# Performance work log

Measured on AMD Instinct MI355X. Metric: run time of the kernel, lower is better.

The kernel has to match this reference:

```python
import jax, jax.numpy as jnp
from jax import lax
import numpy as np

B, T, H, V, C = 64, 64, 1024, 32000, 10
Z, CD = 32, 8  # latent dim, cond embedding dim


def lstm_scan(x_tbh, h0, c0, Wih, Whh, bih, bhh):
    """PyTorch-convention LSTM over time. x_tbh: [T,B,H]; returns hs [T,B,H]."""
    def step(carry, x):
        h, c = carry
        gates = x @ Wih.T + bih + h @ Whh.T + bhh  # [B,4H]
        i, f, g, o = jnp.split(gates, 4, axis=-1)
        c = jax.nn.sigmoid(f) * c + jax.nn.sigmoid(i) * jnp.tanh(g)
        h = jax.nn.sigmoid(o) * jnp.tanh(c)
        return (h, c), h
    _, hs = lax.scan(step, (h0, c0), x_tbh)
    return hs


def setup_inputs() -> dict:
    key = jax.random.key(0)
    ks = jax.random.split(key, 24)
    s = 0.02
    d = {
        'input_word': jax.random.randint(ks[0], (B, T), 0, V),
        'cond': jax.random.randint(ks[1], (B,), 0, C),
        'emb_N': jax.random.normal(ks[2], (V, H), jnp.float32) * s,
        'Wih_N': jax.random.normal(ks[3], (4 * H, H), jnp.float32) * s,
        'Whh_N': jax.random.normal(ks[4], (4 * H, H), jnp.float32) * s,
        'bih_N': jnp.zeros((4 * H,), jnp.float32),
        'bhh_N': jnp.zeros((4 * H,), jnp.float32),
        'emb_D': jax.random.normal(ks[5], (V, H), jnp.float32) * s,
        'Wih_D': jax.random.normal(ks[6], (4 * H, H), jnp.float32) * s,
        'Whh_D': jax.random.normal(ks[7], (4 * H, H), jnp.float32) * s,
        'bih_D': jnp.zeros((4 * H,), jnp.float32),
        'bhh_D': jnp.zeros((4 * H,), jnp.float32),
        'emb_cond': jax.random.normal(ks[8], (C, CD), jnp.float32) * s,
        'W_mean': jax.random.normal(ks[9], (Z, H), jnp.float32) * s,
        'b_mean': jnp.zeros((Z,), jnp.float32),
        'W_logvar': jax.random.normal(ks[10], (Z, H), jnp.float32) * s,
        'b_logvar': jnp.zeros((Z,), jnp.float32),
        'W_st': jax.random.normal(ks[11], (H, Z + CD), jnp.float32) * s,
        'b_st': jnp.zeros((H,), jnp.float32),
        'W_out': jax.random.normal(ks[12], (V, H), jnp.float32) * s,
        'b_out': jnp.zeros((V,), jnp.float32),
        'eps': jax.random.normal(ks[13], (B, Z), jnp.float32),
    }
    return d


def reference(input_word, cond, emb_N, Wih_N, Whh_N, bih_N, bhh_N,
              emb_D, Wih_D, Whh_D, bih_D, bhh_D, emb_cond,
              W_mean, b_mean, W_logvar, b_logvar, W_st, b_st,
              W_out, b_out, eps):
    cond_e = emb_cond[cond]                              # [B,8]
    # ---- encoder ----
    x_enc = jnp.transpose(emb_N[input_word], (1, 0, 2))  # [T,B,H]
    h0 = jnp.concatenate([jnp.zeros((B, H - CD), x_enc.dtype), cond_e], axis=-1)
    c0 = jnp.zeros((B, H), x_enc.dtype)
    hs = lstm_scan(x_enc, h0, c0, Wih_N, Whh_N, bih_N, bhh_N)
    h_t = hs[-1]                                         # [B,H]
    mean_h = h_t @ W_mean.T + b_mean                     # [B,32]
    logvar_h = h_t @ W_logvar.T + b_logvar               # [B,32]
    latent_h = eps * jnp.exp(0.5 * logvar_h) + mean_h    # reparameterize
    # ---- decoder (teacher forcing, start token 0) ----
    hd0 = jnp.concatenate([latent_h, cond_e], axis=-1) @ W_st.T + b_st  # [B,H]
    cd0 = jnp.zeros((B, H), hd0.dtype)
    dec_tok = jnp.concatenate(
        [jnp.zeros((B, 1), input_word.dtype), input_word[:, :-1]], axis=1)
    x_dec = jnp.transpose(emb_D[dec_tok], (1, 0, 2))     # [T,B,H]
    hs_d = lstm_scan(x_dec, hd0, cd0, Wih_D, Whh_D, bih_D, bhh_D)  # [T,B,H]
    logits = hs_d @ W_out.T + b_out                      # [T,B,V]
    return jnp.transpose(logits, (1, 0, 2))              # [B,T,V]
```

## Files before the change

kernel.cpp:

```cpp
#include <hip/hip_runtime.h>
#include <hip/hip_bf16.h>

typedef unsigned short u16;
typedef unsigned int   u32;
typedef unsigned long long u64;
typedef __attribute__((ext_vector_type(8))) short short8;
typedef __attribute__((ext_vector_type(4))) float f32x4;

#define DEVINL static __device__ __forceinline__

DEVINL u16 f2bf(float x) {
  u32 u = __float_as_uint(x);
  u32 r = (u + 0x7fffu + ((u >> 16) & 1u)) >> 16;
  return (u16)r;
}

#define GLD16(gp, lp) __builtin_amdgcn_global_load_lds(                     \
    (const __attribute__((address_space(1))) u32*)(gp),                     \
    (__attribute__((address_space(3))) u32*)(lp), 16, 0, 0)

__global__ __launch_bounds__(256) void conv4(
    const float* __restrict__ s0, u16* __restrict__ d0,
    const float* __restrict__ s1, u16* __restrict__ d1,
    const float* __restrict__ s2, u16* __restrict__ d2,
    const float* __restrict__ s3, u16* __restrict__ d3) {
  int blk = blockIdx.x;
  int p = blk >> 12, local = blk & 4095;
  const float* s = (p == 0) ? s0 : (p == 1) ? s1 : (p == 2) ? s2 : s3;
  u16*         d = (p == 0) ? d0 : (p == 1) ? d1 : (p == 2) ? d2 : d3;
  int i = local * 256 + threadIdx.x;
  float4 v = ((const float4*)s)[i];
  ushort4 o;
  o.x = f2bf(v.x); o.y = f2bf(v.y); o.z = f2bf(v.z); o.w = f2bf(v.w);
  ((ushort4*)d)[i] = o;
}

__global__ __launch_bounds__(256) void conv_wout(const float* __restrict__ s,
                                                 u16* __restrict__ d) {
  int i = blockIdx.x * 256 + threadIdx.x;
  float4 v = ((const float4*)s)[i];
  ushort4 o;
  o.x = f2bf(v.x); o.y = f2bf(v.y); o.z = f2bf(v.z); o.w = f2bf(v.w);
  ((ushort4*)d)[i] = o;
}

__global__ __launch_bounds__(256) void prep_small(
    const int* __restrict__ cond, const float* __restrict__ emb_cond,
    const float* __restrict__ bihN, const float* __restrict__ bhhN,
    const float* __restrict__ bihD, const float* __restrict__ bhhD,
    float* __restrict__ ce, float* __restrict__ biasN, float* __restrict__ biasD,
    u32* __restrict__ bar) {
  int tid = blockIdx.x * 256 + threadIdx.x;
  if (tid < 512) {
    int b = tid >> 3, j = tid & 7;
    ce[tid] = emb_cond[cond[b] * 8 + j];
  }
  int i = tid - 512;
  if (i >= 0 && i < 4096) {
    biasN[i] = bihN[i] + bhhN[i];
    biasD[i] = bihD[i] + bhhD[i];
  }
  int k = tid - 4608;
  if (k >= 0 && k < 1024) bar[k] = 0;
}

__global__ __launch_bounds__(256) void init_enc(const float* __restrict__ ce,
                                                u16* __restrict__ hb0) {
  int tid = blockIdx.x * 256 + threadIdx.x;
  int b = tid >> 10, col = tid & 1023;
  float v = (col >= 1016) ? ce[b * 8 + (col - 1016)] : 0.f;
  hb0[tid] = f2bf(v);
}

__global__ __launch_bounds__(256) void gather_kernel(const float* __restrict__ emb,
                                                     const int* __restrict__ words,
                                                     u16* __restrict__ X, int dec) {
  int r = blockIdx.x;
  int t = r >> 6, b = r & 63;
  int tok = dec ? ((t == 0) ? 0 : words[b * 64 + t - 1]) : words[b * 64 + t];
  float4 v = ((const float4*)(emb + (size_t)tok * 1024))[threadIdx.x];
  ushort4 o;
  o.x = f2bf(v.x); o.y = f2bf(v.y); o.z = f2bf(v.z); o.w = f2bf(v.w);
  ((ushort4*)(X + (size_t)r * 1024))[threadIdx.x] = o;
}

DEVINL void gemm0_body(char* smemc, int bid, int nwg,
                       const u16* __restrict__ A, const u16* __restrict__ B,
                       float* __restrict__ C, const float* __restrict__ bias,
                       int N, int K) {
  u16 (*lA)[256 * 32] = (u16(*)[256 * 32])smemc;
  u16 (*lB)[128 * 32] = (u16(*)[128 * 32])(smemc + 32768);
  const int tid = threadIdx.x;
  const int lane = tid & 63;
  const int wid = tid >> 6;

  const int nn = N >> 7;
  const int wgid = (bid & 7) * (nwg >> 3) + (bid >> 3);
  const int tile_m = (wgid / nn) * 256;
  const int tile_n = (wgid % nn) * 128;
  const int wm = wid >> 1, wn = wid & 1;

  const int ldr = lane >> 2;
  const int lko = (lane & 3) * 8;
  const int l15 = lane & 15;
  const int g4 = lane >> 4;

  const size_t aBase = (size_t)tile_m * K;
  const size_t bBase = (size_t)tile_n * K;

  auto stage = [&](int buf, int k0) {
#pragma unroll
    for (int q = 0; q < 2; ++q) {
      int chk = wid * 2 + q;
      int row = chk * 16 + ldr;
      GLD16(A + aBase + (size_t)row * K + k0 + lko, &lA[buf][chk * 512]);
    }
    int row = wid * 16 + ldr;
    GLD16(B + bBase + (size_t)row * K + k0 + lko, &lB[buf][wid * 512]);
  };

  f32x4 acc[4][4];
#pragma unroll
  for (int i = 0; i < 4; ++i)
#pragma unroll
    for (int j = 0; j < 4; ++j) acc[i][j] = (f32x4)0.f;

  stage(0, 0);
  __syncthreads();

  const int NIT = K >> 5;
  for (int it = 0; it < NIT; ++it) {
    const int cur = it & 1;
    if (it + 1 < NIT) stage(cur ^ 1, (it + 1) * 32);
    short8 af[4], bf[4];
#pragma unroll
    for (int i = 0; i < 4; ++i)
      af[i] = *(const short8*)&lA[cur][(wm * 64 + i * 16 + l15) * 32 + g4 * 8];
#pragma unroll
    for (int j = 0; j < 4; ++j)
      bf[j] = *(const short8*)&lB[cur][(wn * 64 + j * 16 + l15) * 32 + g4 * 8];
#pragma unroll
    for (int i = 0; i < 4; ++i)
#pragma unroll
      for (int j = 0; j < 4; ++j)
        acc[i][j] = __builtin_amdgcn_mfma_f32_16x16x32_bf16(af[i], bf[j], acc[i][j], 0, 0, 0);
    __syncthreads();
  }

#pragma unroll
  for (int i = 0; i < 4; ++i) {
    int row0 = tile_m + wm * 64 + i * 16 + (g4 << 2);
#pragma unroll
    for (int j = 0; j < 4; ++j) {
      int col = tile_n + wn * 64 + j * 16 + l15;
      float bv = bias[col];
#pragma unroll
      for (int e = 0; e < 4; ++e)
        C[(size_t)(row0 + e) * (size_t)N + col] = acc[i][j][e] + bv;
    }
  }
}

DEVINL void lstm_body(char* smemc, const u16* __restrict__ Whh,
                      const float* __restrict__ Xp, u16* __restrict__ hbuf,
                      u16* __restrict__ hs_out, float* __restrict__ hT_out,
                      u32* arrive, u32* prog, int wgi) {
  __builtin_amdgcn_s_setprio(2);
  char* smemA = smemc;
  float (*lg)[16][16] = (float(*)[16][16])(smemc + 32768);
  const int tid = threadIdx.x;
  const int lane = tid & 63;
  const int v = tid >> 6;
  const int gate = v >> 1;
  const int ch = v & 1;
  const int c = wgi >> 5;
  const int j = wgi & 31;
  const int b0 = c * 16, col0 = j * 32;
  const int l15 = lane & 15, g4 = lane >> 4;

  short8 breg[32];
  {
    const u16* Brow = Whh + (size_t)(gate * 1024 + col0 + ch * 16 + l15) * 1024
                          + g4 * 8;
#pragma unroll
    for (int kk = 0; kk < 32; ++kk)
      breg[kk] = *(const short8*)(Brow + kk * 32);
  }

  const int crow = tid >> 5, colw = tid & 31;
  const int bg = b0 + crow, cgl = col0 + colw;
  const int ch2 = colw >> 4, cw = colw & 15;
  float creg = 0.f;

  float xg0, xg1, xg2, xg3;
  {
    size_t xrow = (size_t)bg * 4096 + cgl;
    xg0 = __builtin_nontemporal_load(&Xp[xrow]);
    xg1 = __builtin_nontemporal_load(&Xp[xrow + 1024]);
    xg2 = __builtin_nontemporal_load(&Xp[xrow + 2048]);
    xg3 = __builtin_nontemporal_load(&Xp[xrow + 3072]);
  }

  for (int t = 0; t < 64; ++t) {
    const char* rbase = (const char*)(hbuf + (size_t)(t & 1) * 65536)
                      + (size_t)b0 * 2048;
    u32* wb32 = (u32*)(hbuf + (size_t)((t + 1) & 1) * 65536);

#pragma unroll
    for (int q = 0; q < 4; ++q) {
      int g = q * 512 + tid;
      int row = g >> 7;
      int cb = (g & 127) * 16;
      const u64* src = (const u64*)(rbase + (size_t)row * 2048 + cb);
      u64 lo = __hip_atomic_load(src,     __ATOMIC_RELAXED, __HIP_MEMORY_SCOPE_AGENT);
      u64 hi = __hip_atomic_load(src + 1, __ATOMIC_RELAXED, __HIP_MEMORY_SCOPE_AGENT);
      u64* d = (u64*)(smemA + row * 2048 + (cb ^ ((row & 7) << 4)));
      d[0] = lo; d[1] = hi;
    }
    __syncthreads();

    f32x4 a4[4] = {(f32x4)0.f, (f32x4)0.f, (f32x4)0.f, (f32x4)0.f};
#pragma unroll
    for (int kk = 0; kk < 32; ++kk) {
      int cb2 = kk * 64 + g4 * 16;
      const short8 a = *(const short8*)(smemA + l15 * 2048 + (cb2 ^ ((l15 & 7) << 4)));
      a4[kk & 3] = __builtin_amdgcn_mfma_f32_16x16x32_bf16(a, breg[kk], a4[kk & 3], 0, 0, 0);
    }
    f32x4 asum = a4[0] + a4[1] + a4[2] + a4[3];
    {
      int m = g4 * 4;
#pragma unroll
      for (int e = 0; e < 4; ++e) lg[v][m + e][l15] = asum[e];
    }
    __syncthreads();

    {
      float gi = lg[0 + ch2][crow][cw] + xg0;
      float gf = lg[2 + ch2][crow][cw] + xg1;
      float gg = lg[4 + ch2][crow][cw] + xg2;
      float go = lg[6 + ch2][crow][cw] + xg3;
      float si = 1.f / (1.f + __expf(-gi));
      float sf = 1.f / (1.f + __expf(-gf));
      float so = 1.f / (1.f + __expf(-go));
      float tg = tanhf(gg);
      float cn = sf * creg + si * tg;
      float hn = so * tanhf(cn);
      creg = cn;
      u16 h16 = f2bf(hn);
      u32 mine = h16;
      u32 other = (u32)__shfl_xor((int)mine, 1);
      if (!(colw & 1)) {
        u32 pk = mine | (other << 16);
        __hip_atomic_store(wb32 + (((size_t)bg * 1024 + cgl) >> 1), pk,
                           __ATOMIC_RELAXED, __HIP_MEMORY_SCOPE_AGENT);
        if (hs_out)
          __hip_atomic_store((u32*)hs_out + ((((size_t)t * 64 + bg) * 1024 + cgl) >> 1),
                             pk, __ATOMIC_RELAXED, __HIP_MEMORY_SCOPE_AGENT);
      }
      if (hT_out && t == 63) hT_out[bg * 1024 + cgl] = hn;
    }

    if (t != 63) {
      {
        size_t xrow = (size_t)((t + 1) * 64 + bg) * 4096 + cgl;
        xg0 = __builtin_nontemporal_load(&Xp[xrow]);
        xg1 = __builtin_nontemporal_load(&Xp[xrow + 1024]);
        xg2 = __builtin_nontemporal_load(&Xp[xrow + 2048]);
        xg3 = __builtin_nontemporal_load(&Xp[xrow + 3072]);
      }
      u32 want = (u32)(t + 1);
      asm volatile("s_waitcnt vmcnt(0)" ::: "memory");
      __syncthreads();
      if (tid == 0)
        __hip_atomic_store(&arrive[wgi], want, __ATOMIC_RELAXED,
                           __HIP_MEMORY_SCOPE_AGENT);
      if (tid < 32) {
        int guard = 0;
        while (__hip_atomic_load(&arrive[c * 32 + tid], __ATOMIC_RELAXED,
                                 __HIP_MEMORY_SCOPE_AGENT) < want) {
          __builtin_amdgcn_s_sleep(2);
          if (++guard > (1 << 20)) break;
        }
      }
      __syncthreads();
      if (prog && j == 0 && tid == 0)
        __hip_atomic_store(&prog[c], want, __ATOMIC_RELAXED,
                           __HIP_MEMORY_SCOPE_AGENT);
    }
  }

  if (prog) {
    asm volatile("s_waitcnt vmcnt(0)" ::: "memory");
    __syncthreads();
    if (tid == 0)
      __hip_atomic_store(&arrive[wgi], 64u, __ATOMIC_RELAXED,
                         __HIP_MEMORY_SCOPE_AGENT);
    if (j == 0) {
      if (tid < 32) {
        int guard = 0;
        while (__hip_atomic_load(&arrive[c * 32 + tid], __ATOMIC_RELAXED,
                                 __HIP_MEMORY_SCOPE_AGENT) < 64u) {
          __builtin_amdgcn_s_sleep(2);
          if (++guard > (1 << 20)) break;
        }
      }
      __syncthreads();
      if (tid == 0)
        __hip_atomic_store(&prog[c], 64u, __ATOMIC_RELAXED,
                           __HIP_MEMORY_SCOPE_AGENT);
    }
  }
  __builtin_amdgcn_s_setprio(0);
}

__global__ __launch_bounds__(512, 1) void lstm_cluster(
    const u16* __restrict__ Whh, const float* __restrict__ Xp,
    u16* __restrict__ hbuf, float* __restrict__ hT_out, u32* arrive) {
  __shared__ __align__(16) char smem[40960];
  lstm_body(smem, Whh, Xp, hbuf, nullptr, hT_out, arrive, nullptr, blockIdx.x);
}

__global__ __launch_bounds__(512) void gemm_bt0(
    const u16* __restrict__ A, const u16* __restrict__ B,
    float* __restrict__ C, const float* __restrict__ bias, int N, int K) {
  __shared__ __align__(16) char smem[49152];
  gemm0_body(smem, blockIdx.x, gridDim.x, A, B, C, bias, N, K);
}

__global__ __launch_bounds__(512, 1) void enc_fused(
    const u16* __restrict__ whhN, const float* __restrict__ XpE,
    u16* __restrict__ hbuf, float* __restrict__ hT_out, u32* arrive,
    const u16* __restrict__ Xd, const u16* __restrict__ wihD,
    float* __restrict__ XpD, const float* __restrict__ biasD,
    const float* __restrict__ Wout, u16* __restrict__ wout) {
  __shared__ __align__(16) char smem[49152];
  if (blockIdx.x < 128) {
    lstm_body(smem, whhN, XpE, hbuf, nullptr, hT_out, arrive, nullptr, blockIdx.x);
  } else if (blockIdx.x < 640) {
    gemm0_body(smem, blockIdx.x - 128, 512, Xd, wihD, XpD, biasD, 4096, 1024);
  } else {
    int tid0 = (blockIdx.x - 640) * 512 + threadIdx.x;
    for (int i = tid0; i < 8192000; i += 512 * 512) {
      float4 v = ((const float4*)Wout)[i];
      ushort4 o;
      o.x = f2bf(v.x); o.y = f2bf(v.y); o.z = f2bf(v.z); o.w = f2bf(v.w);
      ((ushort4*)wout)[i] = o;
    }
  }
}

__global__ __launch_bounds__(512, 1) void dec_fused(
    const u16* __restrict__ whhD, const float* __restrict__ XpD,
    u16* __restrict__ hbuf, u16* __restrict__ hsd, u32* arrive, u32* prog,
    const u16* __restrict__ wout, float* __restrict__ out,
    const float* __restrict__ b_out) {
  __shared__ __align__(16) char smem[49152];
  if (blockIdx.x < 128) {
    lstm_body(smem, whhD, XpD, hbuf, hsd, nullptr, arrive, prog, blockIdx.x);
    return;
  }
  u16 (*lA)[256 * 32] = (u16(*)[256 * 32])smem;
  u16 (*lB)[128 * 32] = (u16(*)[128 * 32])(smem + 32768);
  const int tid = threadIdx.x;
  const int lane = tid & 63;
  const int wid = tid >> 6;

  const int i = blockIdx.x - 128;
  const int x = i & 7;
  const int k = i >> 3;
  const int mg = k >> 6;
  const int r  = k & 63;
  const int kn = r >> 1;
  const int mi = r & 1;
  const int tn = kn * 8 + x;
  if (tn >= 250) return;
  const int mt = mg * 2 + mi;
  const int tile_m = mt * 256;
  const int tile_n = tn * 128;
  const int wm = wid >> 1, wn = wid & 1;
  const int N = 32000, K = 1024;

  {
    u32 need = (u32)(mt * 4 + 4);
    if (tid < 4) {
      int guard = 0;
      while (__hip_atomic_load(&prog[tid], __ATOMIC_RELAXED,
                               __HIP_MEMORY_SCOPE_AGENT) < need) {
        __builtin_amdgcn_s_sleep(8);
        if (++guard > (1 << 22)) break;
      }
    }
    __syncthreads();
  }

  const int ldr = lane >> 2;
  const int lko = (lane & 3) * 8;
  const int l15 = lane & 15;
  const int g4 = lane >> 4;

  const size_t aBase = (size_t)tile_m * K;
  const size_t bBase = (size_t)tile_n * K;

  f32x4 acc[4][4];
#pragma unroll
  for (int i2 = 0; i2 < 4; ++i2)
#pragma unroll
    for (int j2 = 0; j2 < 4; ++j2) acc[i2][j2] = (f32x4)0.f;

  auto stg = [&](int buf, int k0) {
#pragma unroll
    for (int q = 0; q < 2; ++q) {
      int chk = wid * 2 + q;
      int row = chk * 16 + ldr;
      GLD16(hsd + aBase + (size_t)row * K + k0 + lko, &lA[buf][chk * 512]);
    }
    int row = wid * 16 + ldr;
    GLD16(wout + bBase + (size_t)row * K + k0 + lko, &lB[buf][wid * 512]);
  };

  stg(0, 0);
  __syncthreads();

  const int NIT = K >> 5;
  for (int it = 0; it < NIT; ++it) {
    const int cur = it & 1;
    if (it + 1 < NIT) stg(cur ^ 1, (it + 1) * 32);
    short8 af[4], bf[4];
#pragma unroll
    for (int i2 = 0; i2 < 4; ++i2)
      af[i2] = *(const short8*)&lA[cur][(wm * 64 + i2 * 16 + l15) * 32 + g4 * 8];
#pragma unroll
    for (int j2 = 0; j2 < 4; ++j2)
      bf[j2] = *(const short8*)&lB[cur][(wn * 64 + j2 * 16 + l15) * 32 + g4 * 8];
#pragma unroll
    for (int i2 = 0; i2 < 4; ++i2)
#pragma unroll
      for (int j2 = 0; j2 < 4; ++j2)
        acc[i2][j2] = __builtin_amdgcn_mfma_f32_16x16x32_bf16(af[i2], bf[j2], acc[i2][j2], 0, 0, 0);
    __syncthreads();
  }

#pragma unroll
  for (int i2 = 0; i2 < 4; ++i2) {
    int row0 = tile_m + wm * 64 + i2 * 16 + (g4 << 2);
#pragma unroll
    for (int j2 = 0; j2 < 4; ++j2) {
      int col = tile_n + wn * 64 + j2 * 16 + l15;
      float bv = b_out[col];
#pragma unroll
      for (int e = 0; e < 4; ++e) {
        int rr = row0 + e;
        size_t o = (size_t)((rr & 63) * 64 + (rr >> 6)) * (size_t)N + col;
        __builtin_nontemporal_store(acc[i2][j2][e] + bv, &out[o]);
      }
    }
  }
}

__global__ __launch_bounds__(256) void latent_hd0_kernel(
    const float* hT, const float* Wm, const float* bm,
    const float* Wl, const float* bl, const float* Wst, const float* bst,
    const float* eps, const float* ce, u16* hb0) {
  __shared__ float red[64][4];
  __shared__ float ml[64];
  __shared__ float lat[40];
  int b = blockIdx.x;
  int tid = threadIdx.x;
  int o = tid >> 2, p = tid & 3;
  const float* w = (o < 32) ? (Wm + (size_t)o * 1024) : (Wl + (size_t)(o - 32) * 1024);
  const float* h = hT + (size_t)b * 1024;
  float s = 0.f;
  for (int k = p * 256; k < p * 256 + 256; ++k) s += h[k] * w[k];
  red[o][p] = s;
  __syncthreads();
  if (tid < 64) {
    float v = red[tid][0] + red[tid][1] + red[tid][2] + red[tid][3];
    v += (tid < 32) ? bm[tid] : bl[tid - 32];
    ml[tid] = v;
  }
  __syncthreads();
  if (tid < 32) lat[tid] = eps[b * 32 + tid] * __expf(0.5f * ml[32 + tid]) + ml[tid];
  if (tid >= 32 && tid < 40) lat[tid] = ce[b * 8 + (tid - 32)];
  __syncthreads();
  for (int hc = tid; hc < 1024; hc += 256) {
    float s2 = bst[hc];
    const float* wr = Wst + (size_t)hc * 40;
#pragma unroll
    for (int j = 0; j < 40; ++j) s2 += lat[j] * wr[j];
    hb0[b * 1024 + hc] = f2bf(s2);
  }
}

extern "C" void kernel_launch(void* const* d_in, const int* in_sizes, int n_in,
                              void* d_out, int out_size, void* d_ws, size_t ws_size,
                              hipStream_t stream) {
  const int*   input_word = (const int*)d_in[0];
  const int*   cond       = (const int*)d_in[1];
  const float* emb_N      = (const float*)d_in[2];
  const float* Wih_N      = (const float*)d_in[3];
  const float* Whh_N      = (const float*)d_in[4];
  const float* bih_N      = (const float*)d_in[5];
  const float* bhh_N      = (const float*)d_in[6];
  const float* emb_D      = (const float*)d_in[7];
  const float* Wih_D      = (const float*)d_in[8];
  const float* Whh_D      = (const float*)d_in[9];
  const float* bih_D      = (const float*)d_in[10];
  const float* bhh_D      = (const float*)d_in[11];
  const float* emb_cond   = (const float*)d_in[12];
  const float* W_mean     = (const float*)d_in[13];
  const float* b_mean     = (const float*)d_in[14];
  const float* W_logvar   = (const float*)d_in[15];
  const float* b_logvar   = (const float*)d_in[16];
  const float* W_st       = (const float*)d_in[17];
  const float* b_st       = (const float*)d_in[18];
  const float* W_out      = (const float*)d_in[19];
  const float* b_out      = (const float*)d_in[20];
  const float* eps        = (const float*)d_in[21];
  float* out = (float*)d_out;

  char* ws = (char*)d_ws;
  size_t off = 0;
  auto alloc = [&](size_t b) { size_t p = off; off += (b + 255) & ~(size_t)255; return p; };
  u16*   wihN = (u16*)(ws + alloc(4096ull * 1024 * 2));
  u16*   whhN = (u16*)(ws + alloc(4096ull * 1024 * 2));
  u16*   wihD = (u16*)(ws + alloc(4096ull * 1024 * 2));
  u16*   whhD = (u16*)(ws + alloc(4096ull * 1024 * 2));
  u16*   wout = (u16*)(ws + alloc(32000ull * 1024 * 2));
  u16*   Xe   = (u16*)(ws + alloc(4096ull * 1024 * 2));
  u16*   Xd   = (u16*)(ws + alloc(4096ull * 1024 * 2));
  float* Xp   = (float*)(ws + alloc(4096ull * 4096 * 4));
  u16*   hsd  = (u16*)(ws + alloc(4096ull * 1024 * 2));
  u16*   hb   = (u16*)(ws + alloc(2ull * 64 * 1024 * 2));
  float* hf   = (float*)(ws + alloc(64ull * 1024 * 4));
  float* biasN = (float*)(ws + alloc(4096 * 4));
  float* biasD = (float*)(ws + alloc(4096 * 4));
  float* ce    = (float*)(ws + alloc(64 * 8 * 4));
  u32*   bar   = (u32*)(ws + alloc(4096));
  size_t base_off = off;
  float* XpD2 = (float*)(ws + alloc(4096ull * 4096 * 4));
  if (base_off > ws_size) return;
  const bool fused = (off <= ws_size);
  float* XpD = fused ? XpD2 : Xp;

  conv4<<<16384, 256, 0, stream>>>(Wih_N, wihN, Whh_N, whhN,
                                   Wih_D, wihD, Whh_D, whhD);
  prep_small<<<22, 256, 0, stream>>>(cond, emb_cond, bih_N, bhh_N, bih_D, bhh_D,
                                     ce, biasN, biasD, bar);
  gather_kernel<<<4096, 256, 0, stream>>>(emb_N, input_word, Xe, 0);
  gather_kernel<<<4096, 256, 0, stream>>>(emb_D, input_word, Xd, 1);
  init_enc<<<256, 256, 0, stream>>>(ce, hb);

  gemm_bt0<<<512, 512, 0, stream>>>(Xe, wihN, Xp, biasN, 4096, 1024);
  if (fused) {
    enc_fused<<<1152, 512, 0, stream>>>(whhN, Xp, hb, hf, bar + 0,
                                        Xd, wihD, XpD, biasD, W_out, wout);
  } else {
    conv_wout<<<32000, 256, 0, stream>>>(W_out, wout);
    lstm_cluster<<<128, 512, 0, stream>>>(whhN, Xp, hb, hf, bar + 0);
  }
  latent_hd0_kernel<<<64, 256, 0, stream>>>(hf, W_mean, b_mean, W_logvar, b_logvar,
                                            W_st, b_st, eps, ce, hb);
  if (!fused)
    gemm_bt0<<<512, 512, 0, stream>>>(Xd, wihD, XpD, biasD, 4096, 1024);
  dec_fused<<<4224, 512, 0, stream>>>(whhD, XpD, hb, hsd, bar + 256, bar + 512,
                                      wout, out, b_out);
}
```

Before: 994.5 us.

## Merge front-end prep kernels into one launch and triple-buffer output GEMM

Five small preprocessing kernels (weight conversion, bias/cond prep, two embedding gathers, encoder h0 init) are folded into one launch that dispatches on block index, which removes several launch gaps. The output-projection GEMM in the decoder kernel moves from double to triple-buffered LDS staging. Each iteration now waits on vmcnt and issues a single barrier, replacing two __syncthreads per iteration. The LDS footprint grows to 72KB per block, which may limit co-residency, and the barrier-reset/hb0 ordering now depends on work within the same launch.

```diff
diff --git a/kernel.cpp b/kernel.cpp
--- a/kernel.cpp
+++ b/kernel.cpp
@@ -19,20 +19,59 @@
     (const __attribute__((address_space(1))) u32*)(gp),                     \
     (__attribute__((address_space(3))) u32*)(lp), 16, 0, 0)
 
-__global__ __launch_bounds__(256) void conv4(
+__global__ __launch_bounds__(256) void front_all(
     const float* __restrict__ s0, u16* __restrict__ d0,
     const float* __restrict__ s1, u16* __restrict__ d1,
     const float* __restrict__ s2, u16* __restrict__ d2,
-    const float* __restrict__ s3, u16* __restrict__ d3) {
+    const float* __restrict__ s3, u16* __restrict__ d3,
+    const int* __restrict__ cond, const float* __restrict__ emb_cond,
+    const float* __restrict__ bihN, const float* __restrict__ bhhN,
+    const float* __restrict__ bihD, const float* __restrict__ bhhD,
+    float* __restrict__ ce, float* __restrict__ biasN, float* __restrict__ biasD,
+    u32* __restrict__ bar,
+    const float* __restrict__ embN, const float* __restrict__ embD,
+    const int* __restrict__ words, u16* __restrict__ Xe, u16* __restrict__ Xd,
+    u16* __restrict__ hb0) {
   int blk = blockIdx.x;
-  int p = blk >> 12, local = blk & 4095;
-  const float* s = (p == 0) ? s0 : (p == 1) ? s1 : (p == 2) ? s2 : s3;
-  u16*         d = (p == 0) ? d0 : (p == 1) ? d1 : (p == 2) ? d2 : d3;
-  int i = local * 256 + threadIdx.x;
-  float4 v = ((const float4*)s)[i];
-  ushort4 o;
-  o.x = f2bf(v.x); o.y = f2bf(v.y); o.z = f2bf(v.z); o.w = f2bf(v.w);
-  ((ushort4*)d)[i] = o;
+  if (blk < 16384) {
+    int p = blk >> 12, local = blk & 4095;
+    const float* s = (p == 0) ? s0 : (p == 1) ? s1 : (p == 2) ? s2 : s3;
+    u16*         d = (p == 0) ? d0 : (p == 1) ? d1 : (p == 2) ? d2 : d3;
+    int i = local * 256 + threadIdx.x;
+    float4 v = ((const float4*)s)[i];
+    ushort4 o;
+    o.x = f2bf(v.x); o.y = f2bf(v.y); o.z = f2bf(v.z); o.w = f2bf(v.w);
+    ((ushort4*)d)[i] = o;
+  } else if (blk < 16406) {
+    int tid = (blk - 16384) * 256 + threadIdx.x;
+    if (tid < 512) {
+      int b = tid >> 3, j = tid & 7;
+      ce[tid] = emb_cond[cond[b] * 8 + j];
+    }
+    int i = tid - 512;
+    if (i >= 0 && i < 4096) {
+      biasN[i] = bihN[i] + bhhN[i];
+      biasD[i] = bihD[i] + bhhD[i];
+    }
+    int k = tid - 4608;
+    if (k >= 0 && k < 1024) bar[k] = 0;
+  } else if (blk < 24598) {
+    int dec = (blk >= 20502);
+    int r = blk - (dec ? 20502 : 16406);
+    int t = r >> 6, b = r & 63;
+    int tok = dec ? ((t == 0) ? 0 : words[b * 64 + t - 1]) : words[b * 64 + t];
+    const float* emb = dec ? embD : embN;
+    u16* X = dec ? Xd : Xe;
+    float4 v = ((const float4*)(emb + (size_t)tok * 1024))[threadIdx.x];
+    ushort4 o;
+    o.x = f2bf(v.x); o.y = f2bf(v.y); o.z = f2bf(v.z); o.w = f2bf(v.w);
+    ((ushort4*)(X + (size_t)r * 1024))[threadIdx.x] = o;
+  } else {
+    int tid = (blk - 24598) * 256 + threadIdx.x;
+    int b = tid >> 10, col = tid & 1023;
+    float v = (col >= 1016) ? emb_cond[cond[b] * 8 + (col - 1016)] : 0.f;
+    hb0[tid] = f2bf(v);
+  }
 }
 
 __global__ __launch_bounds__(256) void conv_wout(const float* __restrict__ s,
@@ -42,46 +81,6 @@
   ushort4 o;
   o.x = f2bf(v.x); o.y = f2bf(v.y); o.z = f2bf(v.z); o.w = f2bf(v.w);
   ((ushort4*)d)[i] = o;
-}
-
-__global__ __launch_bounds__(256) void prep_small(
-    const int* __restrict__ cond, const float* __restrict__ emb_cond,
-    const float* __restrict__ bihN, const float* __restrict__ bhhN,
-    const float* __restrict__ bihD, const float* __restrict__ bhhD,
-    float* __restrict__ ce, float* __restrict__ biasN, float* __restrict__ biasD,
-    u32* __restrict__ bar) {
-  int tid = blockIdx.x * 256 + threadIdx.x;
-  if (tid < 512) {
-    int b = tid >> 3, j = tid & 7;
-    ce[tid] = emb_cond[cond[b] * 8 + j];
-  }
-  int i = tid - 512;
-  if (i >= 0 && i < 4096) {
-    biasN[i] = bihN[i] + bhhN[i];
-    biasD[i] = bihD[i] + bhhD[i];
-  }
-  int k = tid - 4608;
-  if (k >= 0 && k < 1024) bar[k] = 0;
-}
-
-__global__ __launch_bounds__(256) void init_enc(const float* __restrict__ ce,
-                                                u16* __restrict__ hb0) {
-  int tid = blockIdx.x * 256 + threadIdx.x;
-  int b = tid >> 10, col = tid & 1023;
-  float v = (col >= 1016) ? ce[b * 8 + (col - 1016)] : 0.f;
-  hb0[tid] = f2bf(v);
-}
-
-__global__ __launch_bounds__(256) void gather_kernel(const float* __restrict__ emb,
-                                                     const int* __restrict__ words,
-                                                     u16* __restrict__ X, int dec) {
-  int r = blockIdx.x;
-  int t = r >> 6, b = r & 63;
-  int tok = dec ? ((t == 0) ? 0 : words[b * 64 + t - 1]) : words[b * 64 + t];
-  float4 v = ((const float4*)(emb + (size_t)tok * 1024))[threadIdx.x];
-  ushort4 o;
-  o.x = f2bf(v.x); o.y = f2bf(v.y); o.z = f2bf(v.z); o.w = f2bf(v.w);
-  ((ushort4*)(X + (size_t)r * 1024))[threadIdx.x] = o;
 }
 
 DEVINL void gemm0_body(char* smemc, int bid, int nwg,
@@ -354,13 +353,13 @@
     u16* __restrict__ hbuf, u16* __restrict__ hsd, u32* arrive, u32* prog,
     const u16* __restrict__ wout, float* __restrict__ out,
     const float* __restrict__ b_out) {
-  __shared__ __align__(16) char smem[49152];
+  __shared__ __align__(16) char smem[73728];
   if (blockIdx.x < 128) {
     lstm_body(smem, whhD, XpD, hbuf, hsd, nullptr, arrive, prog, blockIdx.x);
     return;
   }
   u16 (*lA)[256 * 32] = (u16(*)[256 * 32])smem;
-  u16 (*lB)[128 * 32] = (u16(*)[128 * 32])(smem + 32768);
+  u16 (*lB)[128 * 32] = (u16(*)[128 * 32])(smem + 49152);
   const int tid = threadIdx.x;
   const int lane = tid & 63;
   const int wid = tid >> 6;
@@ -401,12 +400,6 @@
   const size_t aBase = (size_t)tile_m * K;
   const size_t bBase = (size_t)tile_n * K;
 
-  f32x4 acc[4][4];
-#pragma unroll
-  for (int i2 = 0; i2 < 4; ++i2)
-#pragma unroll
-    for (int j2 = 0; j2 < 4; ++j2) acc[i2][j2] = (f32x4)0.f;
-
   auto stg = [&](int buf, int k0) {
 #pragma unroll
     for (int q = 0; q < 2; ++q) {
@@ -418,13 +411,24 @@
     GLD16(wout + bBase + (size_t)row * K + k0 + lko, &lB[buf][wid * 512]);
   };
 
+  f32x4 acc[4][4];
+#pragma unroll
+  for (int i2 = 0; i2 < 4; ++i2)
+#pragma unroll
+    for (int j2 = 0; j2 < 4; ++j2) acc[i2][j2] = (f32x4)0.f;
+
   stg(0, 0);
-  __syncthreads();
 
   const int NIT = K >> 5;
   for (int it = 0; it < NIT; ++it) {
-    const int cur = it & 1;
-    if (it + 1 < NIT) stg(cur ^ 1, (it + 1) * 32);
+    const int cur = it % 3;
+    if (it + 1 < NIT) {
+      stg((it + 1) % 3, (it + 1) * 32);
+      asm volatile("s_waitcnt vmcnt(3)" ::: "memory");
+    } else {
+      asm volatile("s_waitcnt vmcnt(0)" ::: "memory");
+    }
+    __builtin_amdgcn_s_barrier();
     short8 af[4], bf[4];
 #pragma unroll
     for (int i2 = 0; i2 < 4; ++i2)
@@ -437,7 +441,6 @@
 #pragma unroll
       for (int j2 = 0; j2 < 4; ++j2)
         acc[i2][j2] = __builtin_amdgcn_mfma_f32_16x16x32_bf16(af[i2], bf[j2], acc[i2][j2], 0, 0, 0);
-    __syncthreads();
   }
 
 #pragma unroll
@@ -542,13 +545,12 @@
   const bool fused = (off <= ws_size);
   float* XpD = fused ? XpD2 : Xp;
 
-  conv4<<<16384, 256, 0, stream>>>(Wih_N, wihN, Whh_N, whhN,
-                                   Wih_D, wihD, Whh_D, whhD);
-  prep_small<<<22, 256, 0, stream>>>(cond, emb_cond, bih_N, bhh_N, bih_D, bhh_D,
-                                     ce, biasN, biasD, bar);
-  gather_kernel<<<4096, 256, 0, stream>>>(emb_N, input_word, Xe, 0);
-  gather_kernel<<<4096, 256, 0, stream>>>(emb_D, input_word, Xd, 1);
-  init_enc<<<256, 256, 0, stream>>>(ce, hb);
+  front_all<<<24854, 256, 0, stream>>>(Wih_N, wihN, Whh_N, whhN,
+                                       Wih_D, wihD, Whh_D, whhD,
+                                       cond, emb_cond,
+                                       bih_N, bhh_N, bih_D, bhh_D,
+                                       ce, biasN, biasD, bar,
+                                       emb_N, emb_D, input_word, Xe, Xd, hb);
 
   gemm_bt0<<<512, 512, 0, stream>>>(Xe, wihN, Xp, biasN, 4096, 1024);
   if (fused) {
```

Measured after the change: 940.6 us. 1.06x faster.
